# Kernel optimization log

Hardware: AMD Instinct MI355X
Metric: run time of the kernel (lower is better)

Reference implementation:

```python
import jax, jax.numpy as jnp
import numpy as np
import math

B, H_IM, W_IM, HDIM, HEADS, PS = 16, 56, 56, 512, 8, 7


def setup_inputs() -> dict:
    key = jax.random.key(0)
    ks = jax.random.split(key, 4)
    x = jax.random.normal(ks[0], (B, H_IM * W_IM, HDIM), jnp.float32)
    mask = jnp.zeros((1, 1, H_IM, W_IM), jnp.bool_)
    Wqkv = jax.random.normal(ks[1], (HDIM, 3 * HDIM), jnp.float32) * 0.02
    Wproj = jax.random.normal(ks[2], (HDIM, HDIM), jnp.float32) * 0.02
    bproj = jnp.zeros((HDIM,), jnp.float32)
    rel_bias = jax.random.normal(ks[3], (HEADS, PS * PS, PS * PS), jnp.float32) * 0.02
    return {"x": x, "mask": mask, "Wqkv": Wqkv, "Wproj": Wproj,
            "bproj": bproj, "rel_bias": rel_bias, "H": H_IM, "W": W_IM}


def reference(x, mask, Wqkv, Wproj, bproj, rel_bias, H, W):
    b = x.shape[0]
    ps, g, hd = PS, HEADS, HDIM
    dh = hd // g
    scale = dh ** (-0.5)

    qkv = x @ Wqkv                                   # [b, H*W, 3*hd]
    qkv = qkv.reshape(b, H, W, 3 * hd)
    pad_b = int(math.ceil(H / ps)) * ps - H
    pad_r = int(math.ceil(W / ps)) * ps - W
    qkv = jnp.pad(qkv, ((0, 0), (0, pad_b), (0, pad_r), (0, 0)))
    kmask = jnp.pad(mask, ((0, 0), (0, 0), (0, pad_b), (0, pad_r)), constant_values=True)
    Hp, Wp = H + pad_b, W + pad_r
    sh, sw = Hp // ps, Wp // ps
    K, P = ps * ps, sh * sw

    # patchify: b (sh kh) (sw kw) c -> b (kh kw) (sh sw) c
    qkv = qkv.reshape(b, sh, ps, sw, ps, 3 * hd).transpose(0, 2, 4, 1, 3, 5).reshape(b, K, P, 3 * hd)
    kmask = kmask.reshape(1, 1, sh, ps, sw, ps).transpose(0, 1, 3, 5, 2, 4).reshape(1, 1, K, P)

    qkv = qkv.reshape(b, K, P, 3, g, dh)
    q, k, v = qkv[:, :, :, 0], qkv[:, :, :, 1], qkv[:, :, :, 2]  # each [b, K, P, g, dh]

    attn = jnp.einsum('bqpgc,bkpgc->bgqkp', q, k)    # [b, g, K, K, P]
    attn = (attn + rel_bias[None, :, :, :, None]) * scale
    m = kmask[:, None]                                # [1, 1, 1, K, P]
    attn = jnp.where(m, -jnp.inf, attn)
    attn = jax.nn.softmax(attn, axis=-2)              # softmax over key positions within window
    attn = jnp.where(m, 0.0, attn)

    out = jnp.einsum('bgqkp,bkpgc->bqpgc', attn, v)
    out = out.reshape(b, K, P, hd)
    # un-patchify: b (kh kw) (sh sw) c -> b (sh kh) (sw kw) c
    out = out.reshape(b, ps, ps, sh, sw, hd).transpose(0, 3, 1, 4, 2, 5).reshape(b, Hp, Wp, hd)
    out = out[:, :H, :W, :].reshape(b, H * W, hd)
    return out @ Wproj + bproj
```

## Files before the change

kernel.cpp:

```cpp
#include <hip/hip_runtime.h>
#include <hip/hip_bf16.h>

using bf16 = __hip_bfloat16;
using bf16x8 = __attribute__((ext_vector_type(8))) short;
using f32x4  = __attribute__((ext_vector_type(4))) float;

#define B_    16
#define HIM   56
#define WIM   56
#define HD    512
#define NHEAD 8
#define DH    64
#define NTOK  (HIM*WIM)
#define M_    (B_*NTOK)
#define K49   49

__device__ __forceinline__ void gload_lds16(const void* g, void* l) {
  __builtin_amdgcn_global_load_lds(
      (__attribute__((address_space(1))) const void*)g,
      (__attribute__((address_space(3))) void*)l, 16, 0, 0);
}

__global__ __launch_bounds__(256) void cvt_x_kernel(const float* __restrict__ in,
                                                    bf16* __restrict__ out) {
  size_t i = ((size_t)blockIdx.x * 256 + threadIdx.x) * 8;
  float4 a = *(const float4*)(in + i);
  float4 b = *(const float4*)(in + i + 4);
  union { uint4 v; bf16 h[8]; } o;
  o.h[0] = __float2bfloat16(a.x); o.h[1] = __float2bfloat16(a.y);
  o.h[2] = __float2bfloat16(a.z); o.h[3] = __float2bfloat16(a.w);
  o.h[4] = __float2bfloat16(b.x); o.h[5] = __float2bfloat16(b.y);
  o.h[6] = __float2bfloat16(b.z); o.h[7] = __float2bfloat16(b.w);
  *(uint4*)(out + i) = o.v;
}

__global__ __launch_bounds__(256) void cvt_transpose_kernel(const float* __restrict__ in,
                                                            bf16* __restrict__ out,
                                                            int K, int N) {
  int idx = blockIdx.x * 256 + threadIdx.x;
  int k = idx / N, n = idx - k * N;
  out[(size_t)n * K + k] = __float2bfloat16(in[idx]);
}

template<bool OUT_BF16, bool BIAS>
__global__ __launch_bounds__(512, 2) void gemm256_kernel(
    const bf16* __restrict__ A,
    const bf16* __restrict__ Bt,
    void* __restrict__ Cp,
    const float* __restrict__ bias,
    int M, int N, int K, int NBX)
{
  __shared__ alignas(16) bf16 lds[2][4][256 * 32];
  const int tid  = threadIdx.x;
  const int lane = tid & 63, wid = tid >> 6;
  const int l15  = lane & 15, kq = lane >> 4;
  const int wm   = wid >> 2,  wn = wid & 3;
  const int cpx = gridDim.x >> 3;
  const int wg  = (blockIdx.x & 7) * cpx + (blockIdx.x >> 3);
  const int by  = wg / NBX, bx = wg - by * NBX;
  const long arow0 = (long)by * 256;
  const long bcol0 = (long)bx * 256;

  auto stageHalf = [&](int ab, int j) {
    const bf16* g = (ab ? Bt + bcol0 * K : A + arow0 * K) + j * 32;
    bf16* lbase = &lds[ab][j & 3][0];
#pragma unroll
    for (int c = 0; c < 2; ++c) {
      int s   = c * 512 + tid;
      int row = s >> 2, sl = s & 3;
      int gs  = sl ^ ((row >> 1) & 3);
      gload_lds16((const char*)(g + (long)row * K) + gs * 16,
                  lbase + (c * 512 + wid * 64) * 8);
    }
  };

  f32x4 acc[8][4] = {};

#define KSLICE(J, VM, DOSTAGE) {                                                        \
    const int sl4 = (J) & 3;                                                            \
    asm volatile("s_waitcnt vmcnt(" #VM ")" ::: "memory");                              \
    __builtin_amdgcn_s_barrier();                                                       \
    __builtin_amdgcn_sched_barrier(0);                                                  \
    bf16x8 af[8], bf[2];                                                                \
    _Pragma("unroll")                                                                   \
    for (int mt = 0; mt < 8; ++mt) {                                                    \
      int row = wm * 128 + mt * 16 + l15;                                               \
      af[mt] = *(const bf16x8*)&lds[0][sl4][row * 32 + ((kq ^ ((row >> 1) & 3)) << 3)]; \
    }                                                                                   \
    _Pragma("unroll")                                                                   \
    for (int nt = 0; nt < 2; ++nt) {                                                    \
      int row = wn * 64 + nt * 16 + l15;                                                \
      bf[nt] = *(const bf16x8*)&lds[1][sl4][row * 32 + ((kq ^ ((row >> 1) & 3)) << 3)]; \
    }                                                                                   \
    if (DOSTAGE) stageHalf(0, (J) + 3);                                                 \
    asm volatile("s_waitcnt lgkmcnt(0)" ::: "memory");                                  \
    __builtin_amdgcn_sched_barrier(0);                                                  \
    __builtin_amdgcn_s_setprio(1);                                                      \
    _Pragma("unroll")                                                                   \
    for (int mt = 0; mt < 8; ++mt)                                                      \
      _Pragma("unroll")                                                                 \
      for (int nt = 0; nt < 2; ++nt)                                                    \
        acc[mt][nt] = __builtin_amdgcn_mfma_f32_16x16x32_bf16(bf[nt], af[mt],           \
                                                              acc[mt][nt], 0, 0, 0);    \
    __builtin_amdgcn_s_setprio(0);                                                      \
    __builtin_amdgcn_s_barrier();                                                       \
    bf16x8 bg[2];                                                                       \
    _Pragma("unroll")                                                                   \
    for (int nt = 0; nt < 2; ++nt) {                                                    \
      int row = wn * 64 + (nt + 2) * 16 + l15;                                          \
      bg[nt] = *(const bf16x8*)&lds[1][sl4][row * 32 + ((kq ^ ((row >> 1) & 3)) << 3)]; \
    }                                                                                   \
    if (DOSTAGE) stageHalf(1, (J) + 3);                                                 \
    asm volatile("s_waitcnt lgkmcnt(0)" ::: "memory");                                  \
    __builtin_amdgcn_sched_barrier(0);                                                  \
    __builtin_amdgcn_s_setprio(1);                                                      \
    _Pragma("unroll")                                                                   \
    for (int mt = 0; mt < 8; ++mt)                                                      \
      _Pragma("unroll")                                                                 \
      for (int nt = 0; nt < 2; ++nt)                                                    \
        acc[mt][nt + 2] = __builtin_amdgcn_mfma_f32_16x16x32_bf16(bg[nt], af[mt],       \
                                                              acc[mt][nt + 2], 0, 0, 0);\
    __builtin_amdgcn_s_setprio(0);                                                      \
    __builtin_amdgcn_s_barrier();                                                       \
  }

  stageHalf(0, 0); stageHalf(1, 0);
  stageHalf(0, 1); stageHalf(1, 1);
  stageHalf(0, 2); stageHalf(1, 2);

  const int NK = K >> 5;
#pragma unroll 1
  for (int j = 0; j < NK - 3; ++j) KSLICE(j, 8, true);
  KSLICE(NK - 3, 8, false);
  KSLICE(NK - 2, 4, false);
  KSLICE(NK - 1, 0, false);
#undef KSLICE

  const long crow0 = arow0 + wm * 128;
  const long ccol0 = bcol0 + wn * 64 + kq * 4;
#pragma unroll
  for (int mt = 0; mt < 8; ++mt) {
    long row = crow0 + mt * 16 + l15;
#pragma unroll
    for (int nt = 0; nt < 4; ++nt) {
      long col = ccol0 + nt * 16;
      if (OUT_BF16) {
        union { unsigned long long u; unsigned short h[4]; } pk;
#pragma unroll
        for (int r = 0; r < 4; ++r) {
          bf16 hh = __float2bfloat16(acc[mt][nt][r]);
          pk.h[r] = *(unsigned short*)&hh;
        }
        __builtin_nontemporal_store(pk.u,
            (unsigned long long*)((bf16*)Cp + row * N + col));
      } else {
        f32x4 o = acc[mt][nt];
        if (BIAS) {
          o[0] += bias[col];     o[1] += bias[col + 1];
          o[2] += bias[col + 2]; o[3] += bias[col + 3];
        }
        __builtin_nontemporal_store(o, (f32x4*)((float*)Cp + row * N + col));
      }
    }
  }
}

__global__ __launch_bounds__(256) void attn_win_kernel(
    const bf16* __restrict__ qkv, const float* __restrict__ rb, bf16* __restrict__ outa)
{
  __shared__ alignas(16) bf16 Qs[64 * 72];
  __shared__ alignas(16) bf16 Ks[64 * 72];
  __shared__ alignas(16) bf16 Vt[64 * 72];
  __shared__ alignas(16) bf16 Ps[64 * 72];
  const int tid = threadIdx.x, lane = tid & 63, wid = tid >> 6;
  const int p = blockIdx.x, g = blockIdx.y, b = blockIdx.z;
  const int sh = p >> 3, sw = p & 7;
  const size_t nb = (size_t)b * NTOK;
  const int c8 = (tid & 7) * 8;

#pragma unroll
  for (int it = 0; it < 2; ++it) {
    int t = (tid >> 3) + it * 32;
    uint4 vq = {0, 0, 0, 0}, vk = vq, vv = vq;
    if (t < K49) {
      int ph = t / 7, pw = t - ph * 7;
      int n = (sh * 7 + ph) * WIM + sw * 7 + pw;
      const bf16* src = qkv + (nb + n) * 1536 + g * 64 + c8;
      vq = *(const uint4*)(src);
      vk = *(const uint4*)(src + 512);
      vv = *(const uint4*)(src + 1024);
    }
    *(uint4*)&Qs[t * 72 + c8] = vq;
    *(uint4*)&Ks[t * 72 + c8] = vk;
    union { uint4 u; unsigned short s[8]; } uv; uv.u = vv;
    unsigned short* vt16 = (unsigned short*)Vt;
#pragma unroll
    for (int e = 0; e < 8; ++e) vt16[(c8 + e) * 72 + t] = uv.s[e];
  }
  __syncthreads();

  const int l15 = lane & 15, kq = lane >> 4;
  bf16x8 aq[2];
#pragma unroll
  for (int kk = 0; kk < 2; ++kk)
    aq[kk] = *(const bf16x8*)&Qs[(wid * 16 + l15) * 72 + kk * 32 + kq * 8];
  float sv[4][4];
#pragma unroll
  for (int ct = 0; ct < 4; ++ct) {
    f32x4 acc = {0.f, 0.f, 0.f, 0.f};
#pragma unroll
    for (int kk = 0; kk < 2; ++kk) {
      bf16x8 bk = *(const bf16x8*)&Ks[(ct * 16 + l15) * 72 + kk * 32 + kq * 8];
      acc = __builtin_amdgcn_mfma_f32_16x16x32_bf16(aq[kk], bk, acc, 0, 0, 0);
    }
    int kcol = ct * 16 + l15;
#pragma unroll
    for (int r = 0; r < 4; ++r) {
      int q = wid * 16 + kq * 4 + r;
      float bias = (q < K49 && kcol < K49) ? rb[((size_t)g * K49 + q) * K49 + kcol] : 0.f;
      float v = (acc[r] + bias) * 0.125f;
      sv[ct][r] = (kcol < K49) ? v : -1e30f;
    }
  }
#pragma unroll
  for (int r = 0; r < 4; ++r) {
    float m = fmaxf(fmaxf(sv[0][r], sv[1][r]), fmaxf(sv[2][r], sv[3][r]));
#pragma unroll
    for (int d = 1; d < 16; d <<= 1) m = fmaxf(m, __shfl_xor(m, d));
    float e0 = __expf(sv[0][r] - m), e1 = __expf(sv[1][r] - m);
    float e2 = __expf(sv[2][r] - m), e3 = __expf(sv[3][r] - m);
    float s = e0 + e1 + e2 + e3;
#pragma unroll
    for (int d = 1; d < 16; d <<= 1) s += __shfl_xor(s, d);
    float inv = 1.0f / s;
    int q = wid * 16 + kq * 4 + r;
    Ps[q * 72 +  0 + l15] = __float2bfloat16(e0 * inv);
    Ps[q * 72 + 16 + l15] = __float2bfloat16(e1 * inv);
    Ps[q * 72 + 32 + l15] = __float2bfloat16(e2 * inv);
    Ps[q * 72 + 48 + l15] = __float2bfloat16(e3 * inv);
  }
  __syncthreads();
  bf16x8 ap[2];
#pragma unroll
  for (int kk = 0; kk < 2; ++kk)
    ap[kk] = *(const bf16x8*)&Ps[(wid * 16 + l15) * 72 + kk * 32 + kq * 8];
#pragma unroll
  for (int ct = 0; ct < 4; ++ct) {
    f32x4 acc = {0.f, 0.f, 0.f, 0.f};
#pragma unroll
    for (int kk = 0; kk < 2; ++kk) {
      bf16x8 bv = *(const bf16x8*)&Vt[(ct * 16 + l15) * 72 + kk * 32 + kq * 8];
      acc = __builtin_amdgcn_mfma_f32_16x16x32_bf16(ap[kk], bv, acc, 0, 0, 0);
    }
#pragma unroll
    for (int r = 0; r < 4; ++r) {
      int q = wid * 16 + kq * 4 + r;
      if (q < K49) {
        int ph = q / 7, pw = q - ph * 7;
        int n = (sh * 7 + ph) * WIM + sw * 7 + pw;
        outa[(nb + n) * HD + g * 64 + ct * 16 + l15] = __float2bfloat16(acc[r]);
      }
    }
  }
}

extern "C" void kernel_launch(void* const* d_in, const int* in_sizes, int n_in,
                              void* d_out, int out_size, void* d_ws, size_t ws_size,
                              hipStream_t stream) {
  (void)in_sizes; (void)n_in; (void)out_size;
  const float* x     = (const float*)d_in[0];
  const float* wqkv  = (const float*)d_in[2];
  const float* wproj = (const float*)d_in[3];
  const float* bproj = (const float*)d_in[4];
  const float* rb    = (const float*)d_in[5];

  char* ws = (char*)d_ws;
  bf16* x_bf    = (bf16*)(ws);
  bf16* wqkv_t  = (bf16*)(ws + 51380224);
  bf16* wproj_t = (bf16*)(ws + 52953088);
  bf16* qkv     = (bf16*)(ws + 53477376);
  bf16* attno   = x_bf;
  float* out    = (float*)d_out;
  if (ws_size < 207618048) return;

  cvt_x_kernel<<<dim3(12544), 256, 0, stream>>>(x, x_bf);
  cvt_transpose_kernel<<<dim3(3072), 256, 0, stream>>>(wqkv, wqkv_t, 512, 1536);
  cvt_transpose_kernel<<<dim3(1024), 256, 0, stream>>>(wproj, wproj_t, 512, 512);
  gemm256_kernel<true, false><<<dim3(1176), 512, 0, stream>>>(
      x_bf, wqkv_t, (void*)qkv, nullptr, M_, 1536, 512, 6);
  attn_win_kernel<<<dim3(64, NHEAD, B_), 256, 0, stream>>>(qkv, rb, attno);
  gemm256_kernel<false, true><<<dim3(392), 512, 0, stream>>>(
      attno, wproj_t, (void*)out, bproj, M_, 512, 512, 2);
}
```

Before: 257.8 us.

## Merge GEMM k-slice halves into one barrier per slice with constant LDS slots

```diff
diff --git a/kernel.cpp b/kernel.cpp
--- a/kernel.cpp
+++ b/kernel.cpp
@@ -42,14 +42,16 @@
   out[(size_t)n * K + k] = __float2bfloat16(in[idx]);
 }
 
-template<bool OUT_BF16, bool BIAS>
+template<int N, bool OUT_BF16, bool BIAS>
 __global__ __launch_bounds__(512, 2) void gemm256_kernel(
     const bf16* __restrict__ A,
     const bf16* __restrict__ Bt,
     void* __restrict__ Cp,
     const float* __restrict__ bias,
-    int M, int N, int K, int NBX)
+    int NBX)
 {
+  constexpr int K  = 512;
+  constexpr int NK = K / 32;
   __shared__ alignas(16) bf16 lds[2][4][256 * 32];
   const int tid  = threadIdx.x;
   const int lane = tid & 63, wid = tid >> 6;
@@ -76,64 +78,46 @@
 
   f32x4 acc[8][4] = {};
 
-#define KSLICE(J, VM, DOSTAGE) {                                                        \
-    const int sl4 = (J) & 3;                                                            \
-    asm volatile("s_waitcnt vmcnt(" #VM ")" ::: "memory");                              \
+#define KSLICE(SL, VMSTR, DOSTAGE, JSTAGE) {                                            \
+    asm volatile("s_waitcnt vmcnt(" VMSTR ")" ::: "memory");                            \
     __builtin_amdgcn_s_barrier();                                                       \
-    __builtin_amdgcn_sched_barrier(0);                                                  \
-    bf16x8 af[8], bf[2];                                                                \
+    bf16x8 af[8], bb[4];                                                                \
     _Pragma("unroll")                                                                   \
     for (int mt = 0; mt < 8; ++mt) {                                                    \
       int row = wm * 128 + mt * 16 + l15;                                               \
-      af[mt] = *(const bf16x8*)&lds[0][sl4][row * 32 + ((kq ^ ((row >> 1) & 3)) << 3)]; \
+      af[mt] = *(const bf16x8*)&lds[0][SL][row * 32 + ((kq ^ ((row >> 1) & 3)) << 3)];  \
     }                                                                                   \
     _Pragma("unroll")                                                                   \
-    for (int nt = 0; nt < 2; ++nt) {                                                    \
+    for (int nt = 0; nt < 4; ++nt) {                                                    \
       int row = wn * 64 + nt * 16 + l15;                                                \
-      bf[nt] = *(const bf16x8*)&lds[1][sl4][row * 32 + ((kq ^ ((row >> 1) & 3)) << 3)]; \
+      bb[nt] = *(const bf16x8*)&lds[1][SL][row * 32 + ((kq ^ ((row >> 1) & 3)) << 3)];  \
     }                                                                                   \
-    if (DOSTAGE) stageHalf(0, (J) + 3);                                                 \
-    asm volatile("s_waitcnt lgkmcnt(0)" ::: "memory");                                  \
-    __builtin_amdgcn_sched_barrier(0);                                                  \
+    if (DOSTAGE) { stageHalf(0, JSTAGE); stageHalf(1, JSTAGE); }                        \
     __builtin_amdgcn_s_setprio(1);                                                      \
     _Pragma("unroll")                                                                   \
     for (int mt = 0; mt < 8; ++mt)                                                      \
       _Pragma("unroll")                                                                 \
-      for (int nt = 0; nt < 2; ++nt)                                                    \
-        acc[mt][nt] = __builtin_amdgcn_mfma_f32_16x16x32_bf16(bf[nt], af[mt],           \
+      for (int nt = 0; nt < 4; ++nt)                                                    \
+        acc[mt][nt] = __builtin_amdgcn_mfma_f32_16x16x32_bf16(bb[nt], af[mt],           \
                                                               acc[mt][nt], 0, 0, 0);    \
     __builtin_amdgcn_s_setprio(0);                                                      \
-    __builtin_amdgcn_s_barrier();                                                       \
-    bf16x8 bg[2];                                                                       \
-    _Pragma("unroll")                                                                   \
-    for (int nt = 0; nt < 2; ++nt) {                                                    \
-      int row = wn * 64 + (nt + 2) * 16 + l15;                                          \
-      bg[nt] = *(const bf16x8*)&lds[1][sl4][row * 32 + ((kq ^ ((row >> 1) & 3)) << 3)]; \
-    }                                                                                   \
-    if (DOSTAGE) stageHalf(1, (J) + 3);                                                 \
-    asm volatile("s_waitcnt lgkmcnt(0)" ::: "memory");                                  \
-    __builtin_amdgcn_sched_barrier(0);                                                  \
-    __builtin_amdgcn_s_setprio(1);                                                      \
-    _Pragma("unroll")                                                                   \
-    for (int mt = 0; mt < 8; ++mt)                                                      \
-      _Pragma("unroll")                                                                 \
-      for (int nt = 0; nt < 2; ++nt)                                                    \
-        acc[mt][nt + 2] = __builtin_amdgcn_mfma_f32_16x16x32_bf16(bg[nt], af[mt],       \
-                                                              acc[mt][nt + 2], 0, 0, 0);\
-    __builtin_amdgcn_s_setprio(0);                                                      \
-    __builtin_amdgcn_s_barrier();                                                       \
   }
 
   stageHalf(0, 0); stageHalf(1, 0);
   stageHalf(0, 1); stageHalf(1, 1);
   stageHalf(0, 2); stageHalf(1, 2);
 
-  const int NK = K >> 5;
 #pragma unroll 1
-  for (int j = 0; j < NK - 3; ++j) KSLICE(j, 8, true);
-  KSLICE(NK - 3, 8, false);
-  KSLICE(NK - 2, 4, false);
-  KSLICE(NK - 1, 0, false);
+  for (int jo = 0; jo < NK - 4; jo += 4) {
+    KSLICE(0, "8", true, jo + 3);
+    KSLICE(1, "8", true, jo + 4);
+    KSLICE(2, "8", true, jo + 5);
+    KSLICE(3, "8", true, jo + 6);
+  }
+  KSLICE(0, "8", true,  15);
+  KSLICE(1, "8", false, 0);
+  KSLICE(2, "4", false, 0);
+  KSLICE(3, "0", false, 0);
 #undef KSLICE
 
   const long crow0 = arow0 + wm * 128;
@@ -286,9 +270,9 @@
   cvt_x_kernel<<<dim3(12544), 256, 0, stream>>>(x, x_bf);
   cvt_transpose_kernel<<<dim3(3072), 256, 0, stream>>>(wqkv, wqkv_t, 512, 1536);
   cvt_transpose_kernel<<<dim3(1024), 256, 0, stream>>>(wproj, wproj_t, 512, 512);
-  gemm256_kernel<true, false><<<dim3(1176), 512, 0, stream>>>(
-      x_bf, wqkv_t, (void*)qkv, nullptr, M_, 1536, 512, 6);
+  gemm256_kernel<1536, true, false><<<dim3(1176), 512, 0, stream>>>(
+      x_bf, wqkv_t, (void*)qkv, nullptr, 6);
   attn_win_kernel<<<dim3(64, NHEAD, B_), 256, 0, stream>>>(qkv, rb, attno);
-  gemm256_kernel<false, true><<<dim3(392), 512, 0, stream>>>(
-      attno, wproj_t, (void*)out, bproj, M_, 512, 512, 2);
-}
+  gemm256_kernel<512, false, true><<<dim3(392), 512, 0, stream>>>(
+      attno, wproj_t, (void*)out, bproj, 2);
+}
```

Measured after the change: 256.4 us. Within noise of the previous version (-0.5%).
